# Performance work log

Measured on AMD Instinct MI355X. Metric: run time of the kernel, lower is better.

## Reference

```python
import jax, jax.numpy as jnp
import numpy as np

SEQ_LEN = 4096
D_IN = 1024
D_OUT = 1024


def setup_inputs() -> dict:
    key = jax.random.key(0)
    k_x, k_q, k_k, k_v = jax.random.split(key, 4)
    s = 1.0 / np.sqrt(D_IN)
    return {
        "x": jax.random.normal(k_x, (SEQ_LEN, D_IN), dtype=jnp.float32),
        "W_query": jax.random.normal(k_q, (D_IN, D_OUT), dtype=jnp.float32) * s,
        "W_key": jax.random.normal(k_k, (D_IN, D_OUT), dtype=jnp.float32) * s,
        "W_value": jax.random.normal(k_v, (D_IN, D_OUT), dtype=jnp.float32) * s,
    }


def reference(x, W_query, W_key, W_value):
    # QKV projections (Linear without bias): [S, d_out]
    q = x @ W_query
    k = x @ W_key
    v = x @ W_value
    # Full S x S score matrix, causal mask, scaled softmax
    scores = q @ k.T  # [S, S]
    seq_len = x.shape[0]
    causal = jnp.tril(jnp.ones((seq_len, seq_len), dtype=bool))
    scores = jnp.where(causal, scores, -jnp.inf)
    scale = 1.0 / jnp.sqrt(jnp.asarray(k.shape[-1], dtype=scores.dtype))
    attn = jax.nn.softmax(scores * scale, axis=-1)
    return attn @ v  # [S, d_out]
```

## Files before the change

kernel.cpp:

```cpp
#include <hip/hip_runtime.h>
#include <math.h>

#define SEQ 4096
#define DIM 1024

typedef unsigned short u16;
typedef __attribute__((ext_vector_type(8))) short short8;
typedef __attribute__((ext_vector_type(4))) float floatx4;
typedef __attribute__((ext_vector_type(4))) unsigned short us4;

__device__ __forceinline__ float bf2f(u16 u) {
    union { unsigned int i; float f; } c; c.i = ((unsigned int)u) << 16; return c.f;
}
__device__ __forceinline__ u16 f2bf(float f) {
    union { float f; unsigned int i; } c; c.f = f;
    return (u16)((c.i + 0x7fffu + ((c.i >> 16) & 1u)) >> 16);
}
__device__ __forceinline__ void gload_lds16(const u16* g, u16* l) {
    __builtin_amdgcn_global_load_lds((const __attribute__((address_space(1))) void*)g,
                                     (__attribute__((address_space(3))) void*)l, 16, 0, 0);
}

template <int MODE>
__global__ __launch_bounds__(256) void gemm_nt(const u16* __restrict__ A,
                                               const u16* __restrict__ B,
                                               void* __restrict__ Cv,
                                               u16* __restrict__ VtOut,
                                               float* __restrict__ Lsum,
                                               int lda, int ldb, int ldc, int Kdim,
                                               float scale0) {
    int row0, col0, kbeg = 0, kend = Kdim;
    if (MODE == 1) {
        const int t = blockIdx.x;
        int by = (int)((sqrtf(8.0f * t + 1.0f) - 1.0f) * 0.5f);
        while ((by + 1) * (by + 2) / 2 <= t) ++by;
        while (by * (by + 1) / 2 > t) --by;
        const int bx = t - by * (by + 1) / 2;
        row0 = by * 128;
        col0 = bx * 128;
    } else if (MODE == 2) {
        col0 = blockIdx.x * 128;
        const int y = blockIdx.y;
        const int r = (y < 32) ? (y << 1) : (63 - ((y - 32) << 1));
        row0 = r * 64;
        kbeg = 0;
        kend = row0 + 64;
    } else {
        row0 = blockIdx.y * 128;
        col0 = blockIdx.x * 128;
    }

    __shared__ u16 As[3][(MODE == 2) ? 2048 : 4096];
    __shared__ u16 Bs[3][4096];

    const int tid  = threadIdx.x;
    const int wave = tid >> 6;
    const int lane = tid & 63;
    const int wm = wave & 1;
    const int wn = wave >> 1;

    const int sB0 = wave * 128 + lane;
    const int sB1 = sB0 + 64;
    const int rB0 = sB0 >> 2, qB0 = ((sB0 & 3) ^ ((sB0 >> 3) & 3)) * 8;
    const int rB1 = sB1 >> 2, qB1 = ((sB1 & 3) ^ ((sB1 >> 3) & 3)) * 8;
    const int sA0 = (MODE == 2) ? (wave * 64 + lane) : sB0;
    const int rA0 = sA0 >> 2, qA0 = ((sA0 & 3) ^ ((sA0 >> 3) & 3)) * 8;

    const u16* aP0 = A + (size_t)(row0 + rA0) * lda + kbeg + qA0;
    const u16* aP1 = A + (size_t)(row0 + rB1) * lda + kbeg + qB1;
    const u16* bP0 = B + (size_t)(col0 + rB0) * ldb + kbeg + qB0;
    const u16* bP1 = B + (size_t)(col0 + rB1) * ldb + kbeg + qB1;
    const int lA0 = (MODE == 2) ? wave * 512 : wave * 1024;
    const int lB0 = wave * 1024;

    constexpr int MT = (MODE == 2) ? 2 : 4;
    floatx4 acc[MT][4] = {};
    const int niter = (kend - kbeg) >> 5;
    const int frow = lane & 15;
    const int xq = (((lane >> 4) ^ ((frow >> 1) & 3))) * 8;
    const int mrow0 = (MODE == 2) ? wm * 32 : wm * 64;

    auto stage = [&](int c) {
        gload_lds16(aP0, &As[c][lA0]);
        if constexpr (MODE != 2) gload_lds16(aP1, &As[c][lA0 + 512]);
        gload_lds16(bP0, &Bs[c][lB0]);
        gload_lds16(bP1, &Bs[c][lB0 + 512]);
        aP0 += 32;
        if constexpr (MODE != 2) aP1 += 32;
        bP0 += 32; bP1 += 32;
    };

    stage(0);
    stage(1);

    auto compute_tile = [&](int c) {
        short8 af[MT], bfr[4];
#pragma unroll
        for (int t = 0; t < MT; ++t)
            af[t] = *(const short8*)&As[c][(mrow0 + t * 16 + frow) * 32 + xq];
#pragma unroll
        for (int t = 0; t < 4; ++t)
            bfr[t] = *(const short8*)&Bs[c][(wn * 64 + t * 16 + frow) * 32 + xq];
#pragma unroll
        for (int mt = 0; mt < MT; ++mt)
#pragma unroll
            for (int nt = 0; nt < 4; ++nt)
                acc[mt][nt] = __builtin_amdgcn_mfma_f32_16x16x32_bf16(
                    af[mt], bfr[nt], acc[mt][nt], 0, 0, 0);
    };

    int cur = 0, pre = 2;
    for (int it = 0; it < niter - 2; ++it) {
        if constexpr (MODE == 2)
            asm volatile("s_waitcnt vmcnt(3)\n\ts_barrier" ::: "memory");
        else
            asm volatile("s_waitcnt vmcnt(4)\n\ts_barrier" ::: "memory");
        short8 af[MT], bfr[4];
#pragma unroll
        for (int t = 0; t < MT; ++t)
            af[t] = *(const short8*)&As[cur][(mrow0 + t * 16 + frow) * 32 + xq];
#pragma unroll
        for (int t = 0; t < 4; ++t)
            bfr[t] = *(const short8*)&Bs[cur][(wn * 64 + t * 16 + frow) * 32 + xq];
        stage(pre);
#pragma unroll
        for (int mt = 0; mt < MT; ++mt)
#pragma unroll
            for (int nt = 0; nt < 4; ++nt)
                acc[mt][nt] = __builtin_amdgcn_mfma_f32_16x16x32_bf16(
                    af[mt], bfr[nt], acc[mt][nt], 0, 0, 0);
        cur = (cur == 2) ? 0 : cur + 1;
        pre = (pre == 2) ? 0 : pre + 1;
    }
    if constexpr (MODE == 2)
        asm volatile("s_waitcnt vmcnt(3)\n\ts_barrier" ::: "memory");
    else
        asm volatile("s_waitcnt vmcnt(4)\n\ts_barrier" ::: "memory");
    compute_tile(cur);
    cur = (cur == 2) ? 0 : cur + 1;
    asm volatile("s_waitcnt vmcnt(0)\n\ts_barrier" ::: "memory");
    compute_tile(cur);

    const int cr = (lane >> 4) * 4;
    const int cc = lane & 15;
    if (MODE == 1) {
        u16* dst = (u16*)Cv;
#pragma unroll
        for (int mt = 0; mt < MT; ++mt) {
#pragma unroll
            for (int r = 0; r < 4; ++r) {
                const int grow = row0 + wm * 64 + mt * 16 + cr + r;
                float rowsum = 0.f;
#pragma unroll
                for (int nt = 0; nt < 4; ++nt) {
                    const int gcol = col0 + wn * 64 + nt * 16 + cc;
                    const float e = (gcol <= grow) ? __expf(acc[mt][nt][r]) : 0.f;
                    rowsum += e;
                    dst[(size_t)grow * ldc + gcol] = f2bf(e);
                }
                rowsum += __shfl_xor(rowsum, 1);
                rowsum += __shfl_xor(rowsum, 2);
                rowsum += __shfl_xor(rowsum, 4);
                rowsum += __shfl_xor(rowsum, 8);
                if (cc == 0) atomicAdd(&Lsum[grow], rowsum);
            }
        }
    } else if (MODE == 2) {
        float* O = (float*)Cv;
#pragma unroll
        for (int mt = 0; mt < MT; ++mt)
#pragma unroll
            for (int r = 0; r < 4; ++r) {
                const int grow = row0 + wm * 32 + mt * 16 + cr + r;
                const float invl = __builtin_amdgcn_rcpf(Lsum[grow]);
#pragma unroll
                for (int nt = 0; nt < 4; ++nt) {
                    const int col = col0 + wn * 64 + nt * 16 + cc;
                    O[(size_t)grow * ldc + col] = acc[mt][nt][r] * invl;
                }
            }
    } else if (MODE == 0 && col0 >= 2048) {
#pragma unroll
        for (int mt = 0; mt < MT; ++mt)
#pragma unroll
            for (int nt = 0; nt < 4; ++nt) {
                const int row = row0 + wm * 64 + mt * 16 + cr;
                const int col = (col0 - 2048) + wn * 64 + nt * 16 + cc;
                us4 o = { f2bf(acc[mt][nt][0]), f2bf(acc[mt][nt][1]),
                          f2bf(acc[mt][nt][2]), f2bf(acc[mt][nt][3]) };
                *(us4*)&VtOut[(size_t)col * SEQ + row] = o;
            }
    } else {
        u16* dst = (u16*)Cv;
        const float sc = (col0 < 1024) ? scale0 : 1.0f;
#pragma unroll
        for (int mt = 0; mt < MT; ++mt)
#pragma unroll
            for (int nt = 0; nt < 4; ++nt)
#pragma unroll
                for (int r = 0; r < 4; ++r) {
                    const int row = row0 + wm * 64 + mt * 16 + cr + r;
                    const int col = col0 + wn * 64 + nt * 16 + cc;
                    dst[(size_t)row * ldc + col] = f2bf(acc[mt][nt][r] * sc);
                }
    }
}

__global__ __launch_bounds__(256) void prep(const float* __restrict__ x,
                                            const float* __restrict__ W0,
                                            const float* __restrict__ W1,
                                            const float* __restrict__ W2,
                                            u16* __restrict__ xb,
                                            u16* __restrict__ Wt,
                                            float* __restrict__ Lsum) {
    __shared__ float tile[32][33];
    const int b = blockIdx.x;
    const int tid = threadIdx.x;
    if (b < 4096) {
        const size_t i = ((size_t)b * 256 + tid) * 4;
        const float4 v = *(const float4*)(x + i);
        us4 o = { f2bf(v.x), f2bf(v.y), f2bf(v.z), f2bf(v.w) };
        *(us4*)(xb + i) = o;
    } else if (b < 7168) {
        const int t = b - 4096;
        const int z = t >> 10;
        const int idx = t & 1023;
        const float* W = (z == 0) ? W0 : (z == 1) ? W1 : W2;
        u16* out = Wt + (size_t)z * DIM * DIM;
        const int bx = (idx & 31) * 32;
        const int by = (idx >> 5) * 32;
        const int tx = tid & 31;
        const int ty = (tid >> 5) * 4;
#pragma unroll
        for (int r = 0; r < 4; ++r)
            tile[ty + r][tx] = W[(size_t)(by + ty + r) * DIM + bx + tx];
        __syncthreads();
#pragma unroll
        for (int r = 0; r < 4; ++r)
            out[(size_t)(bx + ty + r) * DIM + by + tx] = f2bf(tile[tx][ty + r]);
    } else {
        const int t = b - 7168;
        *(float4*)(Lsum + (size_t)(t * 256 + tid) * 4) =
            make_float4(0.f, 0.f, 0.f, 0.f);
    }
}

extern "C" void kernel_launch(void* const* d_in, const int* in_sizes, int n_in,
                              void* d_out, int out_size, void* d_ws, size_t ws_size,
                              hipStream_t stream) {
    const float* x  = (const float*)d_in[0];
    const float* Wq = (const float*)d_in[1];
    const float* Wk = (const float*)d_in[2];
    const float* Wv = (const float*)d_in[3];

    u16* xb    = (u16*)d_ws;
    u16* Wt    = xb  + (size_t)SEQ * DIM;
    u16* QK    = Wt  + (size_t)3072 * DIM;
    u16* Vt    = QK  + (size_t)SEQ * 2048;
    u16* E     = Vt  + (size_t)DIM * SEQ;
    float* Lsum = (float*)(E + (size_t)SEQ * SEQ);

    prep<<<7172, 256, 0, stream>>>(x, Wq, Wk, Wv, xb, Wt, Lsum);

    gemm_nt<0><<<dim3(24, 32), 256, 0, stream>>>(
        xb, Wt, QK, Vt, nullptr, DIM, DIM, 2048, DIM, 0.03125f);

    gemm_nt<1><<<528, 256, 0, stream>>>(
        QK, QK + 1024, E, nullptr, Lsum, 2048, 2048, SEQ, DIM, 1.0f);

    gemm_nt<2><<<dim3(8, 64), 256, 0, stream>>>(
        E, Vt, d_out, nullptr, Lsum, SEQ, SEQ, DIM, SEQ, 1.0f);
}
```

Measured before the change: 189.1 us.

## Shrink PV GEMM tiles to 64x64 and remap blocks for causal load balance

The attention-times-V GEMM now uses 64x64 output tiles instead of 64x128, doubling the grid to 1024 blocks. A packed lookup remaps the linear block index so row tiles of varying causal length are interleaved across column groups, aiming to balance the triangular work across CUs and reduce tail imbalance. LDS per block shrinks, which may allow more blocks per CU. The cost is that each block gets less data reuse, so the E matrix is re-read twice as often.

```diff
diff --git a/kernel.cpp b/kernel.cpp
--- a/kernel.cpp
+++ b/kernel.cpp
@@ -29,6 +29,7 @@
                                                float* __restrict__ Lsum,
                                                int lda, int ldb, int ldc, int Kdim,
                                                float scale0) {
+    constexpr bool PV = (MODE == 2);
     int row0, col0, kbeg = 0, kend = Kdim;
     if (MODE == 1) {
         const int t = blockIdx.x;
@@ -39,10 +40,16 @@
         row0 = by * 128;
         col0 = bx * 128;
     } else if (MODE == 2) {
-        col0 = blockIdx.x * 128;
-        const int y = blockIdx.y;
-        const int r = (y < 32) ? (y << 1) : (63 - ((y - 32) << 1));
+        const int lin = blockIdx.x + (blockIdx.y << 4);
+        const int c = lin & 7;
+        const int j = lin >> 3;
+        const int x = j & 15;
+        const int m = j >> 4;
+        const unsigned long long PK = 0x2F3F20301F0F1000ULL;
+        const int base = (int)((PK >> (m * 8)) & 0x3F);
+        const int r = base + ((m & 2) ? -c : c);
         row0 = r * 64;
+        col0 = x * 64;
         kbeg = 0;
         kend = row0 + 64;
     } else {
@@ -50,8 +57,8 @@
         col0 = blockIdx.x * 128;
     }
 
-    __shared__ u16 As[3][(MODE == 2) ? 2048 : 4096];
-    __shared__ u16 Bs[3][4096];
+    __shared__ u16 As[3][PV ? 2048 : 4096];
+    __shared__ u16 Bs[3][PV ? 2048 : 4096];
 
     const int tid  = threadIdx.x;
     const int wave = tid >> 6;
@@ -59,81 +66,82 @@
     const int wm = wave & 1;
     const int wn = wave >> 1;
 
-    const int sB0 = wave * 128 + lane;
+    const int sB0 = (PV ? wave * 64 : wave * 128) + lane;
     const int sB1 = sB0 + 64;
     const int rB0 = sB0 >> 2, qB0 = ((sB0 & 3) ^ ((sB0 >> 3) & 3)) * 8;
     const int rB1 = sB1 >> 2, qB1 = ((sB1 & 3) ^ ((sB1 >> 3) & 3)) * 8;
-    const int sA0 = (MODE == 2) ? (wave * 64 + lane) : sB0;
+    const int sA0 = (PV ? wave * 64 : wave * 128) + lane;
     const int rA0 = sA0 >> 2, qA0 = ((sA0 & 3) ^ ((sA0 >> 3) & 3)) * 8;
 
     const u16* aP0 = A + (size_t)(row0 + rA0) * lda + kbeg + qA0;
     const u16* aP1 = A + (size_t)(row0 + rB1) * lda + kbeg + qB1;
     const u16* bP0 = B + (size_t)(col0 + rB0) * ldb + kbeg + qB0;
     const u16* bP1 = B + (size_t)(col0 + rB1) * ldb + kbeg + qB1;
-    const int lA0 = (MODE == 2) ? wave * 512 : wave * 1024;
-    const int lB0 = wave * 1024;
-
-    constexpr int MT = (MODE == 2) ? 2 : 4;
-    floatx4 acc[MT][4] = {};
+    const int lA0 = PV ? wave * 512 : wave * 1024;
+    const int lB0 = PV ? wave * 512 : wave * 1024;
+
+    constexpr int MT = PV ? 2 : 4;
+    constexpr int NT = PV ? 2 : 4;
+    floatx4 acc[MT][NT] = {};
     const int niter = (kend - kbeg) >> 5;
     const int frow = lane & 15;
     const int xq = (((lane >> 4) ^ ((frow >> 1) & 3))) * 8;
-    const int mrow0 = (MODE == 2) ? wm * 32 : wm * 64;
-
-    auto stage = [&](int c) {
-        gload_lds16(aP0, &As[c][lA0]);
-        if constexpr (MODE != 2) gload_lds16(aP1, &As[c][lA0 + 512]);
-        gload_lds16(bP0, &Bs[c][lB0]);
-        gload_lds16(bP1, &Bs[c][lB0 + 512]);
-        aP0 += 32;
-        if constexpr (MODE != 2) aP1 += 32;
-        bP0 += 32; bP1 += 32;
+    const int mrow0 = PV ? wm * 32 : wm * 64;
+    const int nrow0 = PV ? wn * 32 : wn * 64;
+
+    auto stage = [&](int c_) {
+        gload_lds16(aP0, &As[c_][lA0]);
+        if constexpr (!PV) gload_lds16(aP1, &As[c_][lA0 + 512]);
+        gload_lds16(bP0, &Bs[c_][lB0]);
+        if constexpr (!PV) gload_lds16(bP1, &Bs[c_][lB0 + 512]);
+        aP0 += 32; bP0 += 32;
+        if constexpr (!PV) { aP1 += 32; bP1 += 32; }
     };
 
     stage(0);
     stage(1);
 
-    auto compute_tile = [&](int c) {
-        short8 af[MT], bfr[4];
+    auto compute_tile = [&](int c_) {
+        short8 af[MT], bfr[NT];
 #pragma unroll
         for (int t = 0; t < MT; ++t)
-            af[t] = *(const short8*)&As[c][(mrow0 + t * 16 + frow) * 32 + xq];
-#pragma unroll
-        for (int t = 0; t < 4; ++t)
-            bfr[t] = *(const short8*)&Bs[c][(wn * 64 + t * 16 + frow) * 32 + xq];
-#pragma unroll
-        for (int mt = 0; mt < MT; ++mt)
-#pragma unroll
-            for (int nt = 0; nt < 4; ++nt)
+            af[t] = *(const short8*)&As[c_][(mrow0 + t * 16 + frow) * 32 + xq];
+#pragma unroll
+        for (int t = 0; t < NT; ++t)
+            bfr[t] = *(const short8*)&Bs[c_][(nrow0 + t * 16 + frow) * 32 + xq];
+#pragma unroll
+        for (int mt = 0; mt < MT; ++mt)
+#pragma unroll
+            for (int nt = 0; nt < NT; ++nt)
                 acc[mt][nt] = __builtin_amdgcn_mfma_f32_16x16x32_bf16(
                     af[mt], bfr[nt], acc[mt][nt], 0, 0, 0);
     };
 
     int cur = 0, pre = 2;
     for (int it = 0; it < niter - 2; ++it) {
-        if constexpr (MODE == 2)
-            asm volatile("s_waitcnt vmcnt(3)\n\ts_barrier" ::: "memory");
+        if constexpr (PV)
+            asm volatile("s_waitcnt vmcnt(2)\n\ts_barrier" ::: "memory");
         else
             asm volatile("s_waitcnt vmcnt(4)\n\ts_barrier" ::: "memory");
-        short8 af[MT], bfr[4];
+        short8 af[MT], bfr[NT];
 #pragma unroll
         for (int t = 0; t < MT; ++t)
             af[t] = *(const short8*)&As[cur][(mrow0 + t * 16 + frow) * 32 + xq];
 #pragma unroll
-        for (int t = 0; t < 4; ++t)
-            bfr[t] = *(const short8*)&Bs[cur][(wn * 64 + t * 16 + frow) * 32 + xq];
+        for (int t = 0; t < NT; ++t)
+            bfr[t] = *(const short8*)&Bs[cur][(nrow0 + t * 16 + frow) * 32 + xq];
         stage(pre);
 #pragma unroll
         for (int mt = 0; mt < MT; ++mt)
 #pragma unroll
-            for (int nt = 0; nt < 4; ++nt)
+            for (int nt = 0; nt < NT; ++nt)
                 acc[mt][nt] = __builtin_amdgcn_mfma_f32_16x16x32_bf16(
                     af[mt], bfr[nt], acc[mt][nt], 0, 0, 0);
         cur = (cur == 2) ? 0 : cur + 1;
         pre = (pre == 2) ? 0 : pre + 1;
     }
-    if constexpr (MODE == 2)
-        asm volatile("s_waitcnt vmcnt(3)\n\ts_barrier" ::: "memory");
+    if constexpr (PV)
+        asm volatile("s_waitcnt vmcnt(2)\n\ts_barrier" ::: "memory");
     else
         asm volatile("s_waitcnt vmcnt(4)\n\ts_barrier" ::: "memory");
     compute_tile(cur);
@@ -152,7 +160,7 @@
                 const int grow = row0 + wm * 64 + mt * 16 + cr + r;
                 float rowsum = 0.f;
 #pragma unroll
-                for (int nt = 0; nt < 4; ++nt) {
+                for (int nt = 0; nt < NT; ++nt) {
                     const int gcol = col0 + wn * 64 + nt * 16 + cc;
                     const float e = (gcol <= grow) ? __expf(acc[mt][nt][r]) : 0.f;
                     rowsum += e;
@@ -174,8 +182,8 @@
                 const int grow = row0 + wm * 32 + mt * 16 + cr + r;
                 const float invl = __builtin_amdgcn_rcpf(Lsum[grow]);
 #pragma unroll
-                for (int nt = 0; nt < 4; ++nt) {
-                    const int col = col0 + wn * 64 + nt * 16 + cc;
+                for (int nt = 0; nt < NT; ++nt) {
+                    const int col = col0 + wn * 32 + nt * 16 + cc;
                     O[(size_t)grow * ldc + col] = acc[mt][nt][r] * invl;
                 }
             }
@@ -183,7 +191,7 @@
 #pragma unroll
         for (int mt = 0; mt < MT; ++mt)
 #pragma unroll
-            for (int nt = 0; nt < 4; ++nt) {
+            for (int nt = 0; nt < NT; ++nt) {
                 const int row = row0 + wm * 64 + mt * 16 + cr;
                 const int col = (col0 - 2048) + wn * 64 + nt * 16 + cc;
                 us4 o = { f2bf(acc[mt][nt][0]), f2bf(acc[mt][nt][1]),
@@ -196,7 +204,7 @@
 #pragma unroll
         for (int mt = 0; mt < MT; ++mt)
 #pragma unroll
-            for (int nt = 0; nt < 4; ++nt)
+            for (int nt = 0; nt < NT; ++nt)
 #pragma unroll
                 for (int r = 0; r < 4; ++r) {
                     const int row = row0 + wm * 64 + mt * 16 + cr + r;
@@ -268,6 +276,6 @@
     gemm_nt<1><<<528, 256, 0, stream>>>(
         QK, QK + 1024, E, nullptr, Lsum, 2048, 2048, SEQ, DIM, 1.0f);
 
-    gemm_nt<2><<<dim3(8, 64), 256, 0, stream>>>(
+    gemm_nt<2><<<dim3(16, 64), 256, 0, stream>>>(
         E, Vt, d_out, nullptr, Lsum, SEQ, SEQ, DIM, SEQ, 1.0f);
 }
```

After: 186.8 us. About the same (-1.2%).
